# Optimization experiments

Hardware: AMD Instinct MI355X
Metric: run time of the kernel (lower is better)

Reference implementation:

```python
import jax, jax.numpy as jnp
import numpy as np

MAX_ATOMS = 14  # hard-coded padded atom slots per residue in the original module


def setup_inputs() -> dict:
    key = jax.random.key(0)
    k1, k2, k3 = jax.random.split(key, 3)
    N_RES = 100000
    C = 128  # config.m; OutputLayer(3) emits m channels, fc1 = Linear(14*m, 1)
    feature = jax.random.normal(k1, (N_RES * MAX_ATOMS, C), dtype=jnp.float32)
    atom_num = jax.random.randint(k2, (N_RES,), 0, MAX_ATOMS, dtype=jnp.int32)
    label_binary = jax.random.randint(k3, (N_RES,), 0, 2, dtype=jnp.int32)
    return {"feature": feature, "atom_num": atom_num, "label_binary": label_binary}


def reference(feature, atom_num, label_binary):
    # Ragged gather-to-padded: atoms of residue r live at flat positions
    # [offset[r], offset[r]+atom_num[r]) in `feature`; copy into slot [r, :atom_num[r], :]
    # of a zero-padded [N_res, 14, C] tensor (the original nested Python loop).
    counts = atom_num.astype(jnp.int32)
    offsets = jnp.concatenate([jnp.zeros((1,), jnp.int32), jnp.cumsum(counts)[:-1]])  # [N_res]
    slots = jnp.arange(MAX_ATOMS, dtype=jnp.int32)                                    # [14]
    idx = offsets[:, None] + slots[None, :]                                           # [N_res, 14]
    mask = slots[None, :] < counts[:, None]                                           # [N_res, 14]
    idx = jnp.clip(idx, 0, feature.shape[0] - 1)
    padded = feature[idx] * mask[:, :, None].astype(feature.dtype)                    # [N_res, 14, C]
    aa_feature = padded.reshape(padded.shape[0], -1)                                  # [N_res, 14*C]
    return aa_feature, label_binary
```

## Files before the change

### kernel.cpp

```cpp
#include <hip/hip_runtime.h>


#define MAX_ATOMS 14
#define CCH 128
#define F4_PER_ROW 32
#define F4_PER_RES (MAX_ATOMS * F4_PER_ROW)
#define RPB 16
#define ITERS ((RPB * F4_PER_RES) / 256)

typedef float f32x4 __attribute__((ext_vector_type(4)));

__global__ void k_local_scan(const int* __restrict__ atom_num, int n,
                             int* __restrict__ local_off,
                             int* __restrict__ sums) {
    __shared__ int lds[256];
    int t = threadIdx.x;
    int r = blockIdx.x * 256 + t;
    int v = (r < n) ? atom_num[r] : 0;
    lds[t] = v;
    __syncthreads();
    for (int d = 1; d < 256; d <<= 1) {
        int add = (t >= d) ? lds[t - d] : 0;
        __syncthreads();
        lds[t] += add;
        __syncthreads();
    }
    if (r < n) local_off[r] = lds[t] - v;
    if (t == 255) sums[blockIdx.x] = lds[255];
}

__global__ void k_scan_sums(int* __restrict__ sums, int nb) {
    __shared__ int lds[512];
    int t = threadIdx.x;
    int v = (t < nb) ? sums[t] : 0;
    lds[t] = v;
    __syncthreads();
    for (int d = 1; d < 512; d <<= 1) {
        int add = (t >= d) ? lds[t - d] : 0;
        __syncthreads();
        lds[t] += add;
        __syncthreads();
    }
    if (t < nb) sums[t] = lds[t] - v;
}

__global__ __launch_bounds__(256) void k_gather(
        const f32x4* __restrict__ feat,
        const int* __restrict__ atom_num,
        const int* __restrict__ local_off,
        const int* __restrict__ block_base,
        const int* __restrict__ label,
        f32x4* __restrict__ out,
        float* __restrict__ out_label,
        int n) {
    __shared__ int off_s[RPB];
    __shared__ int cnt_s[RPB];
    int t = threadIdx.x;
    int rbase = blockIdx.x * RPB;
    if (t < RPB) {
        int r = rbase + t;
        if (r < n) {
            off_s[t] = block_base[rbase >> 8] + local_off[r];
            cnt_s[t] = atom_num[r];
            out_label[r] = (float)label[r];
        } else {
            off_s[t] = 0;
            cnt_s[t] = 0;
        }
    }
    __syncthreads();

    if (rbase + RPB <= n) {
        #pragma unroll 7
        for (int i = 0; i < ITERS; ++i) {
            int e    = t + i * 256;
            int rl   = e / F4_PER_RES;
            int rem  = e - rl * F4_PER_RES;
            int slot = rem >> 5;
            f32x4 val = (f32x4)0.f;
            if (slot < cnt_s[rl]) {
                val = __builtin_nontemporal_load(
                    &feat[(size_t)(off_s[rl] + slot) * F4_PER_ROW + (rem & 31)]);
            }
            __builtin_nontemporal_store(val,
                &out[(size_t)rbase * F4_PER_RES + e]);
        }
    } else {
        for (int i = 0; i < ITERS; ++i) {
            int e    = t + i * 256;
            int rl   = e / F4_PER_RES;
            int rem  = e - rl * F4_PER_RES;
            int slot = rem >> 5;
            if (rbase + rl < n) {
                f32x4 val = (f32x4)0.f;
                if (slot < cnt_s[rl]) {
                    val = __builtin_nontemporal_load(
                        &feat[(size_t)(off_s[rl] + slot) * F4_PER_ROW + (rem & 31)]);
                }
                __builtin_nontemporal_store(val,
                    &out[(size_t)rbase * F4_PER_RES + e]);
            }
        }
    }
}

extern "C" void kernel_launch(void* const* d_in, const int* in_sizes, int n_in,
                              void* d_out, int out_size, void* d_ws, size_t ws_size,
                              hipStream_t stream) {
    const float* feature = (const float*)d_in[0];
    const int* atom_num  = (const int*)d_in[1];
    const int* label     = (const int*)d_in[2];
    const int n = in_sizes[1];

    float* out = (float*)d_out;
    float* out_label = out + (size_t)n * MAX_ATOMS * CCH;

    int* ws_local = (int*)d_ws;
    int* ws_sums  = ws_local + n;

    int nb = (n + 255) / 256;
    k_local_scan<<<nb, 256, 0, stream>>>(atom_num, n, ws_local, ws_sums);
    k_scan_sums<<<1, 512, 0, stream>>>(ws_sums, nb);

    int gb = (n + RPB - 1) / RPB;
    k_gather<<<gb, 256, 0, stream>>>((const f32x4*)feature, atom_num,
                                     ws_local, ws_sums, label,
                                     (f32x4*)out, out_label, n);
}
```

Measured before the change: 219.6 us.

## Fuse offset scan into gather kernel via per-block reduction of chunk sums

Replaces the two-kernel scan (local scan plus single-block scan of sums) with one reduction kernel that only writes per-256-residue chunk sums. Each gather block then sums all preceding chunk sums and the preceding in-chunk atom counts with an LDS tree reduction, and does a small serial prefix over its 16 residues. This drops one kernel launch and the per-residue offset array traffic. In exchange, every gather block does redundant reduction work over up to about 391 chunk sums plus two extra barriers before issuing loads.

```diff
diff --git a/kernel.cpp b/kernel.cpp
--- a/kernel.cpp
+++ b/kernel.cpp
@@ -10,63 +10,59 @@
 
 typedef float f32x4 __attribute__((ext_vector_type(4)));
 
-__global__ void k_local_scan(const int* __restrict__ atom_num, int n,
-                             int* __restrict__ local_off,
-                             int* __restrict__ sums) {
+__global__ __launch_bounds__(256) void k_sums(const int* __restrict__ atom_num,
+                                              int n, int* __restrict__ sums) {
     __shared__ int lds[256];
     int t = threadIdx.x;
     int r = blockIdx.x * 256 + t;
-    int v = (r < n) ? atom_num[r] : 0;
-    lds[t] = v;
+    lds[t] = (r < n) ? atom_num[r] : 0;
     __syncthreads();
-    for (int d = 1; d < 256; d <<= 1) {
-        int add = (t >= d) ? lds[t - d] : 0;
-        __syncthreads();
-        lds[t] += add;
+    for (int d = 128; d > 0; d >>= 1) {
+        if (t < d) lds[t] += lds[t + d];
         __syncthreads();
     }
-    if (r < n) local_off[r] = lds[t] - v;
-    if (t == 255) sums[blockIdx.x] = lds[255];
-}
-
-__global__ void k_scan_sums(int* __restrict__ sums, int nb) {
-    __shared__ int lds[512];
-    int t = threadIdx.x;
-    int v = (t < nb) ? sums[t] : 0;
-    lds[t] = v;
-    __syncthreads();
-    for (int d = 1; d < 512; d <<= 1) {
-        int add = (t >= d) ? lds[t - d] : 0;
-        __syncthreads();
-        lds[t] += add;
-        __syncthreads();
-    }
-    if (t < nb) sums[t] = lds[t] - v;
+    if (t == 0) sums[blockIdx.x] = lds[0];
 }
 
 __global__ __launch_bounds__(256) void k_gather(
         const f32x4* __restrict__ feat,
         const int* __restrict__ atom_num,
-        const int* __restrict__ local_off,
-        const int* __restrict__ block_base,
+        const int* __restrict__ sums,
         const int* __restrict__ label,
         f32x4* __restrict__ out,
         float* __restrict__ out_label,
         int n) {
+    __shared__ int red[256];
     __shared__ int off_s[RPB];
     __shared__ int cnt_s[RPB];
     int t = threadIdx.x;
     int rbase = blockIdx.x * RPB;
+    int c      = rbase >> 8;
+    int j0     = rbase & 255;
+    int chunk0 = c << 8;
+
+    int part = 0;
+    for (int j = t; j < c; j += 256) part += sums[j];
+    if (t < j0) part += atom_num[chunk0 + t];
+    red[t] = part;
+    __syncthreads();
+    for (int d = 128; d > 0; d >>= 1) {
+        if (t < d) red[t] += red[t + d];
+        __syncthreads();
+    }
+    int base = red[0];
+
     if (t < RPB) {
         int r = rbase + t;
-        if (r < n) {
-            off_s[t] = block_base[rbase >> 8] + local_off[r];
-            cnt_s[t] = atom_num[r];
-            out_label[r] = (float)label[r];
-        } else {
-            off_s[t] = 0;
-            cnt_s[t] = 0;
-        }
+        cnt_s[t] = (r < n) ? atom_num[r] : 0;
+        if (r < n) out_label[r] = (float)label[r];
+    }
+    __syncthreads();
+    if (t < RPB) {
+        int o = base;
+        #pragma unroll
+        for (int i = 0; i < RPB; ++i) o += (i < t) ? cnt_s[i] : 0;
+        off_s[t] = o;
     }
     __syncthreads();
 
@@ -115,15 +111,13 @@
     float* out = (float*)d_out;
     float* out_label = out + (size_t)n * MAX_ATOMS * CCH;
 
-    int* ws_local = (int*)d_ws;
-    int* ws_sums  = ws_local + n;
+    int* ws_sums = (int*)d_ws;
 
     int nb = (n + 255) / 256;
-    k_local_scan<<<nb, 256, 0, stream>>>(atom_num, n, ws_local, ws_sums);
-    k_scan_sums<<<1, 512, 0, stream>>>(ws_sums, nb);
+    k_sums<<<nb, 256, 0, stream>>>(atom_num, n, ws_sums);
 
     int gb = (n + RPB - 1) / RPB;
     k_gather<<<gb, 256, 0, stream>>>((const f32x4*)feature, atom_num,
-                                     ws_local, ws_sums, label,
+                                     ws_sums, label,
                                      (f32x4*)out, out_label, n);
 }
```

Result: no change. 218.3 us (-0.6%).
